# Performance work log

Hardware: AMD Instinct MI355X
Metric: run time of the kernel (lower is better)

Reference implementation:

```python
import jax, jax.numpy as jnp
import numpy as np
import math

B, S, D, H = 4, 2048, 1024, 16
HD = D // H  # 64
MOD_DIMS = [("text", 768, 2048), ("image", 1024, 1024), ("audio", 512, 1500), ("video", 2048, 512)]
M = len(MOD_DIMS)
WIN, DEPTH = 3, 8


def _cantor_routes():
    coords = []
    for i in range(M):
        x = i / max(1, M - 1)
        x = max(1e-06, min(x, 1.0 - 1e-06))
        val, f = 0.0, 0.5
        for _ in range(DEPTH):
            x *= 3.0
            d = int(x)
            x -= d
            if d == 2:
                val += f
            f *= 0.5
        coords.append(val)
    c = np.asarray(coords, dtype=np.float32)
    dist = np.abs(c[:, None] - c[None, :])
    # topk smallest distances (stable tie-break like torch ascending sort)
    return np.argsort(dist, axis=1, kind="stable")[:, :WIN]

ROUTES = jnp.asarray(_cantor_routes())


def setup_inputs() -> dict:
    key = jax.random.key(0)
    ks = iter(jax.random.split(key, 32))
    inp = {}
    for name, dim, sl in MOD_DIMS:
        inp[name] = jax.random.normal(next(ks), (B, sl, dim), dtype=jnp.float32)
        inp[f"W_{name}"] = jax.random.normal(next(ks), (D, dim), dtype=jnp.float32) / math.sqrt(dim)
        inp[f"b_{name}"] = jnp.zeros((D,), dtype=jnp.float32)
    inp["mod_emb"] = jax.random.normal(next(ks), (M, D), dtype=jnp.float32) * 0.02
    for nm in ("q", "k", "v", "o"):
        inp[f"W{nm}"] = jax.random.normal(next(ks), (D, D), dtype=jnp.float32) / math.sqrt(D)
        inp[f"b{nm}"] = jnp.zeros((D,), dtype=jnp.float32)
    inp["temperature"] = jnp.asarray(0.07, dtype=jnp.float32)
    return inp


def reference(text, image, audio, video, W_text, b_text, W_image, b_image,
              W_audio, b_audio, W_video, b_video, mod_emb, Wq, bq, Wk, bk,
              Wv, bv, Wo, bo, temperature):
    xs = [text, image, audio, video]
    Ws = [W_text, W_image, W_audio, W_video]
    bs = [b_text, b_image, b_audio, b_video]
    projected = []
    for i in range(M):
        p = xs[i] @ Ws[i].T + bs[i] + mod_emb[i]          # [B, s_i, D]
        p = jnp.pad(p, ((0, 0), (0, S - p.shape[1]), (0, 0)))
        projected.append(p)
    stacked = jnp.stack(projected, axis=1)                # [B, M, S, D]

    def heads(x, W, b):
        return (x @ W.T + b).reshape(B, M, S, H, HD).transpose(0, 3, 1, 2, 4)  # [B,H,M,S,HD]

    Q = heads(stacked, Wq, bq)
    K = heads(stacked, Wk, bk)
    V = heads(stacked, Wv, bv)

    Kn = K[:, :, ROUTES]
    Vn = V[:, :, ROUTES]
    scores = jnp.einsum('bhmsd,bhmwsd->bhmsw', Q, Kn) / (math.sqrt(HD) * jnp.abs(temperature))
    attn = jax.nn.softmax(scores, axis=-1)                # dropout is identity at eval
    out = jnp.einsum('bhmsw,bhmwsd->bhmsd', attn, Vn)     # [B,H,M,S,HD]
    fused = out.mean(axis=2)                              # [B,H,S,HD]
    fused = fused.transpose(0, 2, 1, 3).reshape(B, S, D)
    return fused @ Wo.T + bo
```

## Files before the change

kernel.cpp:

```cpp
#include <hip/hip_runtime.h>

typedef unsigned short u16;
typedef __bf16 bf16x8 __attribute__((ext_vector_type(8)));
typedef u16   u16x8  __attribute__((ext_vector_type(8)));
typedef u16   u16x4  __attribute__((ext_vector_type(4)));
typedef float f32x4  __attribute__((ext_vector_type(4)));

#define RPB 5084
#define SL0 2048
#define SL1 1024
#define SL2 1500
#define SL3 512

__device__ __forceinline__ u16 f2bf(float f) {
  union { float f; unsigned u; } x; x.f = f;
  unsigned u = x.u;
  u += 0x7fffu + ((u >> 16) & 1u);
  return (u16)(u >> 16);
}
__device__ __forceinline__ float bf2f(u16 h) {
  union { unsigned u; float f; } x; x.u = ((unsigned)h) << 16;
  return x.f;
}
__device__ __forceinline__ void gll16(const u16* g, u16* l) {
  __builtin_amdgcn_global_load_lds(
      (const __attribute__((address_space(1))) void*)g,
      (__attribute__((address_space(3))) void*)l, 16, 0, 0);
}


#define NSEG 8
struct CvtSegs {
  const float* src[NSEG];
  u16*         dst[NSEG];
  int          blk_end[NSEG];
  int          blk_base[NSEG];
};
__global__ __launch_bounds__(256) void cvt_multi(CvtSegs segs) {
  int blk = blockIdx.x, seg = 0;
#pragma unroll
  for (int s = 0; s < NSEG; ++s) if (blk >= segs.blk_end[s]) seg = s + 1;
  const float* src = segs.src[seg];
  u16* dst = segs.dst[seg];
  int i = (blk - segs.blk_base[seg]) * 1024 + threadIdx.x * 4;
  f32x4 v = *(const f32x4*)(src + i);
  u16x4 o;
  o[0] = f2bf(v[0]); o[1] = f2bf(v[1]); o[2] = f2bf(v[2]); o[3] = f2bf(v[3]);
  *(u16x4*)(dst + i) = o;
}

struct TrSegs { const float* src[4]; u16* dst[4]; int dimc[4]; int blk_end[4]; };
__global__ __launch_bounds__(256) void cvt_transpose(TrSegs ts) {
  __shared__ float t[32][33];
  int blk = blockIdx.x, seg = 0;
#pragma unroll
  for (int s = 0; s < 3; ++s) if (blk >= ts.blk_end[s]) seg = s + 1;
  int base  = seg ? ts.blk_end[seg - 1] : 0;
  int local = blk - base;
  int DIMc  = ts.dimc[seg];
  int tpr   = DIMc >> 5;
  int tr = local / tpr, tc = local - tr * tpr;
  const float* src = ts.src[seg];
  u16* dst = ts.dst[seg];
  int r0 = tr * 32, c0 = tc * 32;
  int cx = threadIdx.x & 31, ry = threadIdx.x >> 5;
#pragma unroll
  for (int k = 0; k < 4; ++k)
    t[ry + 8 * k][cx] = src[(size_t)(r0 + ry + 8 * k) * DIMc + c0 + cx];
  __syncthreads();
#pragma unroll
  for (int k = 0; k < 4; ++k)
    dst[(size_t)(c0 + ry + 8 * k) * 1024 + r0 + cx] = f2bf(t[cx][ry + 8 * k]);
}

__global__ __launch_bounds__(256) void bias_prep(
    const float* __restrict__ Wq, const float* __restrict__ Wk, const float* __restrict__ Wv,
    const float* __restrict__ bq, const float* __restrict__ bk, const float* __restrict__ bv,
    const float* __restrict__ bm0, const float* __restrict__ bm1,
    const float* __restrict__ bm2, const float* __restrict__ bm3,
    const float* __restrict__ emb, float* __restrict__ out )
{
  const int wid  = blockIdx.x * 4 + (threadIdx.x >> 6);
  const int lane = threadIdx.x & 63;
  const int m = wid / 3072, n = wid - m * 3072;
  const float* wr_ = (n < 1024) ? Wq + (size_t)n * 1024
                   : (n < 2048) ? Wk + (size_t)(n - 1024) * 1024
                                : Wv + (size_t)(n - 2048) * 1024;
  const float  br  = (n < 1024) ? bq[n] : (n < 2048) ? bk[n - 1024] : bv[n - 2048];
  const float* bmp = (m == 0) ? bm0 : (m == 1) ? bm1 : (m == 2) ? bm2 : bm3;
  const float* ep  = emb + (size_t)m * 1024;
  const int k0 = lane * 16;
  float s = 0.f;
#pragma unroll
  for (int i = 0; i < 16; ++i) s += wr_[k0 + i] * (bmp[k0 + i] + ep[k0 + i]);
  s += __shfl_xor(s, 1);  s += __shfl_xor(s, 2);  s += __shfl_xor(s, 4);
  s += __shfl_xor(s, 8);  s += __shfl_xor(s, 16); s += __shfl_xor(s, 32);
  if (lane == 0) out[(size_t)m * 3072 + n] = s + br;
}

struct WpSegs { const u16* Bw[4]; u16* Cout[4]; int Nn[4]; int blk_end[4]; };
__global__ __launch_bounds__(256) void gemm_wprep(WpSegs wsg, const u16* __restrict__ A) {
  int blk = blockIdx.x, seg = 0;
#pragma unroll
  for (int s = 0; s < 3; ++s) if (blk >= wsg.blk_end[s]) seg = s + 1;
  const int base  = seg ? wsg.blk_end[seg - 1] : 0;
  const int local = blk - base;
  const int Nn  = wsg.Nn[seg];
  const int ctm = Nn >> 7;
  const int rt  = local / ctm;
  const int row0 = rt * 128, col0 = (local - rt * ctm) * 128;
  const int K = 1024;
  const u16* Bw = wsg.Bw[seg];
  u16* Cout = wsg.Cout[seg];

  __shared__ u16 lA0[128 * 32], lA1[128 * 32];
  __shared__ u16 lB0[128 * 32], lB1[128 * 32];
  const int tid  = threadIdx.x;
  const int lane = tid & 63;
  const int wave = tid >> 6;
  const int wr   = (wave >> 1) * 64;
  const int wc   = (wave & 1) * 64;

  const int srow = lane >> 2;
  const int soct = (((lane & 3) ^ ((lane >> 3) & 3))) << 3;
  const u16* pA0 = A + (size_t)(row0 + wave * 32 + srow) * K + soct;
  const u16* pA1 = pA0 + (size_t)16 * K;
  const u16* pB0 = Bw + (size_t)(col0 + wave * 32 + srow) * K + soct;
  const u16* pB1 = pB0 + (size_t)16 * K;
  u16* dA0a = &lA0[(wave * 32) * 32];      u16* dA1a = &lA0[(wave * 32 + 16) * 32];
  u16* dA0b = &lA1[(wave * 32) * 32];      u16* dA1b = &lA1[(wave * 32 + 16) * 32];
  u16* dB0a = &lB0[(wave * 32) * 32];      u16* dB1a = &lB0[(wave * 32 + 16) * 32];
  u16* dB0b = &lB1[(wave * 32) * 32];      u16* dB1b = &lB1[(wave * 32 + 16) * 32];

  f32x4 acc[4][4];
#pragma unroll
  for (int i = 0; i < 4; ++i)
#pragma unroll
    for (int j = 0; j < 4; ++j) acc[i][j] = f32x4{0.f, 0.f, 0.f, 0.f};

  const int fr  = lane & 15;
  const int fo  = lane >> 4;
  const int lrd = fr * 32 + (((fo ^ ((fr >> 1) & 3))) << 3);
  const int ca  = (wr >> 4) * 512;
  const int cbb = (wc >> 4) * 512;

  for (int k0 = 0; k0 < K; k0 += 64) {
    __syncthreads();
    gll16(pA0 + k0, dA0a);       gll16(pA1 + k0, dA1a);
    gll16(pB0 + k0, dB0a);       gll16(pB1 + k0, dB1a);
    gll16(pA0 + k0 + 32, dA0b);  gll16(pA1 + k0 + 32, dA1b);
    gll16(pB0 + k0 + 32, dB0b);  gll16(pB1 + k0 + 32, dB1b);
    __syncthreads();

    bf16x8 af[4], bfr[4];
#pragma unroll
    for (int j = 0; j < 4; ++j)
      bfr[j] = *(const bf16x8*)&lB0[cbb + j * 512 + lrd];
#pragma unroll
    for (int i = 0; i < 4; ++i)
      af[i] = *(const bf16x8*)&lA0[ca + i * 512 + lrd];
#pragma unroll
    for (int i = 0; i < 4; ++i)
#pragma unroll
      for (int j = 0; j < 4; ++j)
        acc[i][j] = __builtin_amdgcn_mfma_f32_16x16x32_bf16(af[i], bfr[j], acc[i][j], 0, 0, 0);
#pragma unroll
    for (int j = 0; j < 4; ++j)
      bfr[j] = *(const bf16x8*)&lB1[cbb + j * 512 + lrd];
#pragma unroll
    for (int i = 0; i < 4; ++i)
      af[i] = *(const bf16x8*)&lA1[ca + i * 512 + lrd];
#pragma unroll
    for (int i = 0; i < 4; ++i)
#pragma unroll
      for (int j = 0; j < 4; ++j)
        acc[i][j] = __builtin_amdgcn_mfma_f32_16x16x32_bf16(af[i], bfr[j], acc[i][j], 0, 0, 0);
  }

  const int fc = lane & 15;
  const int rq = (lane >> 4) * 4;
#pragma unroll
  for (int i = 0; i < 4; ++i) {
#pragma unroll
    for (int j = 0; j < 4; ++j) {
      const int gc = col0 + wc + j * 16 + fc;
#pragma unroll
      for (int reg = 0; reg < 4; ++reg) {
        int gr = row0 + wr + i * 16 + rq + reg;
        Cout[(size_t)gr * Nn + gc] = f2bf(acc[i][j][reg]);
      }
    }
  }
}

template<int STORE_F32>
__global__ __launch_bounds__(256) void gemm_lds(
    const u16* __restrict__ A,
    const u16* __restrict__ B0, const u16* __restrict__ B1, const u16* __restrict__ B2,
    const float* __restrict__ c0, const float* __restrict__ c1, const float* __restrict__ c2,
    void* __restrict__ Cout, int Mr, int K, int ldc)
{
  __shared__ u16 lA0[128 * 32], lA1[128 * 32];
  __shared__ u16 lB0[128 * 32], lB1[128 * 32];
  const int tid  = threadIdx.x;
  const int lane = tid & 63;
  const int wave = tid >> 6;
  const int wr   = (wave >> 1) * 64;
  const int wc   = (wave & 1) * 64;
  const int row0 = blockIdx.y * 128;

  const int wsel = blockIdx.x >> 3;
  const int colL = (blockIdx.x & 7) * 128;
  const u16*   Bw   = (wsel == 0) ? B0 : (wsel == 1) ? B1 : B2;
  const float* bias = (wsel == 0) ? c0 : (wsel == 1) ? c1 : c2;

  const int srow = lane >> 2;
  const int soct = (((lane & 3) ^ ((lane >> 3) & 3))) << 3;
  int ra0 = row0 + wave * 32 + srow;      if (ra0 >= Mr) ra0 = Mr - 1;
  int ra1 = row0 + wave * 32 + srow + 16; if (ra1 >= Mr) ra1 = Mr - 1;
  const u16* pA0 = A + (size_t)ra0 * K + soct;
  const u16* pA1 = A + (size_t)ra1 * K + soct;
  const u16* pB0 = Bw + (size_t)(colL + wave * 32 + srow) * K + soct;
  const u16* pB1 = pB0 + (size_t)16 * K;
  u16* dA0a = &lA0[(wave * 32) * 32];      u16* dA1a = &lA0[(wave * 32 + 16) * 32];
  u16* dA0b = &lA1[(wave * 32) * 32];      u16* dA1b = &lA1[(wave * 32 + 16) * 32];
  u16* dB0a = &lB0[(wave * 32) * 32];      u16* dB1a = &lB0[(wave * 32 + 16) * 32];
  u16* dB0b = &lB1[(wave * 32) * 32];      u16* dB1b = &lB1[(wave * 32 + 16) * 32];

  f32x4 acc[4][4];
#pragma unroll
  for (int i = 0; i < 4; ++i)
#pragma unroll
    for (int j = 0; j < 4; ++j) acc[i][j] = f32x4{0.f, 0.f, 0.f, 0.f};

  const int fr  = lane & 15;
  const int fo  = lane >> 4;
  const int lrd = fr * 32 + (((fo ^ ((fr >> 1) & 3))) << 3);
  const int ca  = (wr >> 4) * 512;
  const int cbb = (wc >> 4) * 512;

  for (int k0 = 0; k0 < K; k0 += 64) {
    __syncthreads();
    gll16(pA0 + k0, dA0a);       gll16(pA1 + k0, dA1a);
    gll16(pB0 + k0, dB0a);       gll16(pB1 + k0, dB1a);
    gll16(pA0 + k0 + 32, dA0b);  gll16(pA1 + k0 + 32, dA1b);
    gll16(pB0 + k0 + 32, dB0b);  gll16(pB1 + k0 + 32, dB1b);
    __syncthreads();

    bf16x8 af[4], bfr[4];
#pragma unroll
    for (int j = 0; j < 4; ++j)
      bfr[j] = *(const bf16x8*)&lB0[cbb + j * 512 + lrd];
#pragma unroll
    for (int i = 0; i < 4; ++i)
      af[i] = *(const bf16x8*)&lA0[ca + i * 512 + lrd];
#pragma unroll
    for (int i = 0; i < 4; ++i)
#pragma unroll
      for (int j = 0; j < 4; ++j)
        acc[i][j] = __builtin_amdgcn_mfma_f32_16x16x32_bf16(af[i], bfr[j], acc[i][j], 0, 0, 0);
#pragma unroll
    for (int j = 0; j < 4; ++j)
      bfr[j] = *(const bf16x8*)&lB1[cbb + j * 512 + lrd];
#pragma unroll
    for (int i = 0; i < 4; ++i)
      af[i] = *(const bf16x8*)&lA1[ca + i * 512 + lrd];
#pragma unroll
    for (int i = 0; i < 4; ++i)
#pragma unroll
      for (int j = 0; j < 4; ++j)
        acc[i][j] = __builtin_amdgcn_mfma_f32_16x16x32_bf16(af[i], bfr[j], acc[i][j], 0, 0, 0);
  }

  const int fc = lane & 15;
  const int rq = (lane >> 4) * 4;
#pragma unroll
  for (int i = 0; i < 4; ++i) {
#pragma unroll
    for (int j = 0; j < 4; ++j) {
      const int cl = wc + j * 16 + fc;
      const float badd = bias[colL + cl];
      const int gc = blockIdx.x * 128 + cl;
#pragma unroll
      for (int reg = 0; reg < 4; ++reg) {
        int gr = row0 + wr + i * 16 + rq + reg;
        if (gr < Mr) {
          float v = acc[i][j][reg] + badd;
          if (STORE_F32) ((float*)Cout)[(size_t)gr * ldc + gc] = v;
          else           ((u16*)Cout)[(size_t)gr * ldc + gc] = f2bf(v);
        }
      }
    }
  }
}

struct QkvSegs {
  const u16*   A[4];
  const u16*   Bw[4];
  const float* bias[4];
  int Mr[4], K[4], sl[4], obase[4], blk_end[4];
};
__global__ __launch_bounds__(512, 2) void gemm_qkv_seg(QkvSegs qs, u16* __restrict__ C) {
  __shared__ u16 lds[4][2][8192];
  int blk = blockIdx.x, seg = 0;
#pragma unroll
  for (int s = 0; s < 3; ++s) if (blk >= qs.blk_end[s]) seg = s + 1;
  const int base  = seg ? qs.blk_end[seg - 1] : 0;
  const int local = blk - base;
  const int cbt   = local % 12;
  const int row0  = (local / 12) * 256;
  const int colL  = cbt * 256;
  const int Mr = qs.Mr[seg], K = qs.K[seg], sl = qs.sl[seg], obase = qs.obase[seg];
  const u16* A  = qs.A[seg];
  const u16* Bw = qs.Bw[seg];
  const float* bias = qs.bias[seg];

  const int tid  = threadIdx.x;
  const int lane = tid & 63;
  const int wave = tid >> 6;
  const int wm   = wave >> 2;
  const int wn   = wave & 3;

  const int srow = lane >> 2;
  const int soct = (((lane & 3) ^ ((lane >> 3) & 3))) << 3;
  int ra0 = row0 + wave * 16 + srow;        if (ra0 >= Mr) ra0 = Mr - 1;
  int ra1 = row0 + 128 + wave * 16 + srow;  if (ra1 >= Mr) ra1 = Mr - 1;
  const u16* pA0 = A + (size_t)ra0 * K + soct;
  const u16* pA1 = A + (size_t)ra1 * K + soct;
  const u16* pB0 = Bw + (size_t)(colL + wave * 16 + srow) * K + soct;
  const u16* pB1 = pB0 + (size_t)128 * K;
  const int NS = K >> 5;

#define QSTAGE(slot, k0) do {                                   \
    gll16(pA0 + (k0), (u16*)&lds[slot][0][wave * 512]);         \
    gll16(pA1 + (k0), (u16*)&lds[slot][0][4096 + wave * 512]);  \
    gll16(pB0 + (k0), (u16*)&lds[slot][1][wave * 512]);         \
    gll16(pB1 + (k0), (u16*)&lds[slot][1][4096 + wave * 512]);  \
  } while (0)

  f32x4 acc[8][4];
#pragma unroll
  for (int m = 0; m < 8; ++m)
#pragma unroll
    for (int n = 0; n < 4; ++n) acc[m][n] = f32x4{0.f, 0.f, 0.f, 0.f};

  QSTAGE(0, 0);
  QSTAGE(1, 32);
  QSTAGE(2, 64);

  const int fr  = lane & 15;
  const int fo  = lane >> 4;
  const int lrd = fr * 32 + (((fo ^ ((fr >> 1) & 3))) << 3);
  const int cam = wm * 8 * 512;
  const int cbn = wn * 4 * 512;

#pragma unroll 4
  for (int s = 0; s < NS; ++s) {
    asm volatile("s_waitcnt vmcnt(8)" ::: "memory");
    __builtin_amdgcn_s_barrier();
    asm volatile("" ::: "memory");

    const u16* Ab = &lds[s & 3][0][0];
    const u16* Bb = &lds[s & 3][1][0];
    bf16x8 af[8], bf[4];
#pragma unroll
    for (int n = 0; n < 4; ++n)
      bf[n] = *(const bf16x8*)&Bb[cbn + n * 512 + lrd];
#pragma unroll
    for (int m = 0; m < 8; ++m)
      af[m] = *(const bf16x8*)&Ab[cam + m * 512 + lrd];

    const int s3 = s + 3;
    const int k3 = (s3 < NS ? s3 : NS - 1) << 5;
    QSTAGE(s3 & 3, k3);

#pragma unroll
    for (int m = 0; m < 8; ++m)
#pragma unroll
      for (int n = 0; n < 4; ++n)
        acc[m][n] = __builtin_amdgcn_mfma_f32_16x16x32_bf16(af[m], bf[n], acc[m][n], 0, 0, 0);
  }
#undef QSTAGE

  asm volatile("s_waitcnt vmcnt(0)" ::: "memory");

  const int fc = lane & 15;
  const int rq = (lane >> 4) * 4;
#pragma unroll
  for (int m = 0; m < 8; ++m) {
#pragma unroll
    for (int n = 0; n < 4; ++n) {
      const int cl = wn * 64 + n * 16 + fc;
      const float badd = bias[colL + cl];
      const int gc = colL + cl;
#pragma unroll
      for (int reg = 0; reg < 4; ++reg) {
        int gr = row0 + wm * 128 + m * 16 + rq + reg;
        if (gr < Mr) {
          int bb = gr / sl, ss = gr - bb * sl;
          C[(size_t)(bb * RPB + obase + ss) * 3072 + gc] = f2bf(acc[m][n][reg] + badd);
        }
      }
    }
  }
}

__global__ __launch_bounds__(256) void attn_fuse(
    const u16* __restrict__ QKV,
    u16* __restrict__ fused,
    const float* __restrict__ bq, const float* __restrict__ bk, const float* __restrict__ bv,
    const float* __restrict__ temp_ptr)
{
  const int ROUTE[4][3] = {{0,1,2},{0,1,2},{2,3,0},{3,2,0}};
  const int SLm[4]  = {SL0, SL1, SL2, SL3};
  const int OFFS[4] = {0, 2048, 3072, 4572};
  const int tid  = threadIdx.x;
  const int lane = tid & 63;
  const int wave = tid >> 6;
  const int bs   = blockIdx.x * 2 + (wave >> 1);
  const int s    = bs & 2047;
  const int b    = bs >> 11;
  const int h    = (wave & 1) * 8 + (lane >> 3);
  const int sub  = lane & 7;
  const int dbase = h * 64 + sub * 8;
  const float scale = 1.0f / (8.0f * fabsf(temp_ptr[0]));

  float qf[4][8], kf[4][8], vf[4][8];
#pragma unroll
  for (int r = 0; r < 4; ++r) {
    if (s < SLm[r]) {
      const u16* base = QKV + ((size_t)(b * RPB + OFFS[r] + s)) * 3072 + dbase;
      u16x8 q8 = *(const u16x8*)(base);
      u16x8 k8 = *(const u16x8*)(base + 1024);
      u16x8 v8 = *(const u16x8*)(base + 2048);
#pragma unroll
      for (int i = 0; i < 8; ++i) {
        qf[r][i] = bf2f(q8[i]); kf[r][i] = bf2f(k8[i]); vf[r][i] = bf2f(v8[i]);
      }
    } else {
#pragma unroll
      for (int i = 0; i < 8; ++i) {
        qf[r][i] = bq[dbase + i]; kf[r][i] = bk[dbase + i]; vf[r][i] = bv[dbase + i];
      }
    }
  }

  float acc[8];
#pragma unroll
  for (int i = 0; i < 8; ++i) acc[i] = 0.f;

#pragma unroll
  for (int m = 0; m < 4; ++m) {
    float sc[3];
#pragma unroll
    for (int w = 0; w < 3; ++w) {
      const int r = ROUTE[m][w];
      float d = 0.f;
#pragma unroll
      for (int i = 0; i < 8; ++i) d += qf[m][i] * kf[r][i];
      d += __shfl_xor(d, 1, 64);
      d += __shfl_xor(d, 2, 64);
      d += __shfl_xor(d, 4, 64);
      sc[w] = d * scale;
    }
    float mx = fmaxf(sc[0], fmaxf(sc[1], sc[2]));
    float e0 = __expf(sc[0] - mx), e1 = __expf(sc[1] - mx), e2 = __expf(sc[2] - mx);
    float inv = 1.0f / (e0 + e1 + e2);
    float ws[3] = {e0 * inv, e1 * inv, e2 * inv};
#pragma unroll
    for (int w = 0; w < 3; ++w) {
      const int r = ROUTE[m][w];
#pragma unroll
      for (int i = 0; i < 8; ++i) acc[i] += ws[w] * vf[r][i];
    }
  }
  u16x8 o;
#pragma unroll
  for (int i = 0; i < 8; ++i) o[i] = f2bf(acc[i] * 0.25f);
  *(u16x8*)(fused + (size_t)bs * 1024 + dbase) = o;
}

extern "C" void kernel_launch(void* const* d_in, const int* in_sizes, int n_in,
                              void* d_out, int out_size, void* d_ws, size_t ws_size,
                              hipStream_t stream) {
  const int B = 4, S = 2048, D = 1024;
  const int SL[4]   = {SL0, SL1, SL2, SL3};
  const int DIM[4]  = {768, 1024, 512, 2048};
  const int OFFS[4] = {0, 2048, 3072, 4572};

  const float* x[4]  = {(const float*)d_in[0], (const float*)d_in[3], (const float*)d_in[6], (const float*)d_in[9]};
  const float* Wm[4] = {(const float*)d_in[1], (const float*)d_in[4], (const float*)d_in[7], (const float*)d_in[10]};
  const float* bm[4] = {(const float*)d_in[2], (const float*)d_in[5], (const float*)d_in[8], (const float*)d_in[11]};
  const float* mod_emb = (const float*)d_in[12];
  const float* Wq = (const float*)d_in[13]; const float* bq = (const float*)d_in[14];
  const float* Wk = (const float*)d_in[15]; const float* bk = (const float*)d_in[16];
  const float* Wv = (const float*)d_in[17]; const float* bv = (const float*)d_in[18];
  const float* Wo = (const float*)d_in[19]; const float* bo = (const float*)d_in[20];
  const float* temp = (const float*)d_in[21];

  const int RROWS = B * RPB;
  const size_t qkvB   = ((size_t)RROWS * 3 * D * 2 + 255) / 256 * 256;
  size_t xbB[4], wmTB[4], wqkvmB[4];
  size_t xbTot = 0, wmTTot = 0, wqkvmTot = 0;
  for (int m = 0; m < 4; ++m) {
    xbB[m]    = ((size_t)B * SL[m] * DIM[m] * 2 + 255) / 256 * 256;  xbTot    += xbB[m];
    wmTB[m]   = ((size_t)DIM[m] * D * 2 + 255) / 256 * 256;          wmTTot   += wmTB[m];
    wqkvmB[m] = ((size_t)3 * D * DIM[m] * 2 + 255) / 256 * 256;      wqkvmTot += wqkvmB[m];
  }
  const size_t wB   = (size_t)D * D * 2;
  const size_t bqmB = ((size_t)4 * 3 * D * 4 + 255) / 256 * 256;
  const size_t need = qkvB + xbTot + wmTTot + 3 * wB + wB + wqkvmTot + bqmB;
  if (ws_size < need) return;

  char* p = (char*)d_ws;
  u16* qkv = (u16*)p;  p += qkvB;
  u16* xb[4];
  char* xbBase = p;
  for (int m = 0; m < 4; ++m) { xb[m] = (u16*)p; p += xbB[m]; }
  u16* wmT[4];
  for (int m = 0; m < 4; ++m) { wmT[m] = (u16*)p; p += wmTB[m]; }
  u16* wqb = (u16*)p;  p += wB;
  u16* wkb = (u16*)p;  p += wB;
  u16* wvb = (u16*)p;  p += wB;
  u16* wob = (u16*)p;  p += wB;
  u16* wqkvm[4];
  for (int m = 0; m < 4; ++m) { wqkvm[m] = (u16*)p; p += wqkvmB[m]; }
  float* bqm = (float*)p;  p += bqmB;
  u16* fusedb = (u16*)xbBase;

  {
    CvtSegs cs;
    const float* srcs[NSEG] = {x[0], x[1], x[2], x[3], Wq, Wk, Wv, Wo};
    u16* dsts[NSEG] = {xb[0], xb[1], xb[2], xb[3], wqb, wkb, wvb, wob};
    int ns[NSEG];
    for (int m = 0; m < 4; ++m) ns[m] = B * SL[m] * DIM[m];
    for (int i = 0; i < 4; ++i) ns[4 + i] = D * D;
    int base = 0;
    for (int i = 0; i < NSEG; ++i) {
      cs.src[i] = srcs[i]; cs.dst[i] = dsts[i];
      cs.blk_base[i] = base;
      base += (ns[i] + 1023) / 1024;
      cs.blk_end[i] = base;
    }
    cvt_multi<<<base, 256, 0, stream>>>(cs);
  }

  {
    TrSegs ts;
    int base = 0;
    for (int m = 0; m < 4; ++m) {
      ts.src[m] = Wm[m]; ts.dst[m] = wmT[m]; ts.dimc[m] = DIM[m];
      base += (D / 32) * (DIM[m] / 32);
      ts.blk_end[m] = base;
    }
    cvt_transpose<<<base, 256, 0, stream>>>(ts);
  }

  bias_prep<<<3072, 256, 0, stream>>>(Wq, Wk, Wv, bq, bk, bv,
                                      bm[0], bm[1], bm[2], bm[3], mod_emb, bqm);

  {
    const int ord[4] = {3, 1, 0, 2};
    WpSegs wsg;
    int base = 0;
    for (int i = 0; i < 4; ++i) {
      int m = ord[i];
      wsg.Bw[i] = wmT[m]; wsg.Cout[i] = wqkvm[m]; wsg.Nn[i] = DIM[m];
      base += (3 * D / 128) * (DIM[m] / 128);
      wsg.blk_end[i] = base;
    }
    gemm_wprep<<<base, 256, 0, stream>>>(wsg, wqb);
  }

  {
    const int ord[4] = {3, 1, 0, 2};
    QkvSegs qsg;
    int base = 0;
    for (int i = 0; i < 4; ++i) {
      int m = ord[i];
      int Mr = B * SL[m];
      qsg.A[i] = xb[m]; qsg.Bw[i] = wqkvm[m]; qsg.bias[i] = bqm + m * 3072;
      qsg.Mr[i] = Mr; qsg.K[i] = DIM[m]; qsg.sl[i] = SL[m]; qsg.obase[i] = OFFS[m];
      base += 12 * ((Mr + 255) / 256);
      qsg.blk_end[i] = base;
    }
    gemm_qkv_seg<<<base, 512, 0, stream>>>(qsg, qkv);
  }

  attn_fuse<<<(B * S) / 2, 256, 0, stream>>>(qkv, fusedb, bq, bk, bv, temp);

  {
    dim3 grid(8, (B * S) / 128);
    gemm_lds<1><<<grid, 256, 0, stream>>>(fusedb, wob, wob, wob, bo, bo, bo,
                                          d_out, B * S, D, D);
  }
}
```

Before: 469.7 us.

## Merge prep kernels into one launch and run QKV GEMM with 1024-thread blocks

Three preprocessing kernels (fp32→bf16 conversion, weight transpose, bias folding) become one segmented launch, removing two kernel launches and the gaps between them. The QKV GEMM keeps its 256x256 tile but now uses 16 waves of 1024 threads. Each wave owns a 64x64 sub-tile and issues half as many global→LDS loads per stage, which cuts per-thread accumulators and registers. The epilogue computes the batch/sequence split once per wave instead of dividing per element. The risk is that 1024-thread blocks with 64KB of LDS allow fewer resident blocks per CU and add barrier cost, which may weaken latency hiding in the pipelined K loop.

```diff
diff --git a/kernel.cpp b/kernel.cpp
--- a/kernel.cpp
+++ b/kernel.cpp
@@ -29,73 +29,69 @@
 }
 
 
-#define NSEG 8
-struct CvtSegs {
-  const float* src[NSEG];
-  u16*         dst[NSEG];
-  int          blk_end[NSEG];
-  int          blk_base[NSEG];
+struct PrepAll {
+  const float* csrc[8]; u16* cdst[8]; int cend[8]; int cbase[8];
+  const float* tsrc[4]; u16* tdst[4]; int tdim[4]; int tend[4];
+  const float *Wq, *Wk, *Wv, *bq, *bk, *bv, *bm0, *bm1, *bm2, *bm3, *emb;
+  float* bout;
+  int cvtN, trN;
 };
-__global__ __launch_bounds__(256) void cvt_multi(CvtSegs segs) {
-  int blk = blockIdx.x, seg = 0;
-#pragma unroll
-  for (int s = 0; s < NSEG; ++s) if (blk >= segs.blk_end[s]) seg = s + 1;
-  const float* src = segs.src[seg];
-  u16* dst = segs.dst[seg];
-  int i = (blk - segs.blk_base[seg]) * 1024 + threadIdx.x * 4;
-  f32x4 v = *(const f32x4*)(src + i);
-  u16x4 o;
-  o[0] = f2bf(v[0]); o[1] = f2bf(v[1]); o[2] = f2bf(v[2]); o[3] = f2bf(v[3]);
-  *(u16x4*)(dst + i) = o;
-}
-
-struct TrSegs { const float* src[4]; u16* dst[4]; int dimc[4]; int blk_end[4]; };
-__global__ __launch_bounds__(256) void cvt_transpose(TrSegs ts) {
+__global__ __launch_bounds__(256) void prep_all(PrepAll pa) {
   __shared__ float t[32][33];
-  int blk = blockIdx.x, seg = 0;
-#pragma unroll
-  for (int s = 0; s < 3; ++s) if (blk >= ts.blk_end[s]) seg = s + 1;
-  int base  = seg ? ts.blk_end[seg - 1] : 0;
-  int local = blk - base;
-  int DIMc  = ts.dimc[seg];
-  int tpr   = DIMc >> 5;
-  int tr = local / tpr, tc = local - tr * tpr;
-  const float* src = ts.src[seg];
-  u16* dst = ts.dst[seg];
-  int r0 = tr * 32, c0 = tc * 32;
-  int cx = threadIdx.x & 31, ry = threadIdx.x >> 5;
-#pragma unroll
-  for (int k = 0; k < 4; ++k)
-    t[ry + 8 * k][cx] = src[(size_t)(r0 + ry + 8 * k) * DIMc + c0 + cx];
-  __syncthreads();
-#pragma unroll
-  for (int k = 0; k < 4; ++k)
-    dst[(size_t)(c0 + ry + 8 * k) * 1024 + r0 + cx] = f2bf(t[cx][ry + 8 * k]);
-}
-
-__global__ __launch_bounds__(256) void bias_prep(
-    const float* __restrict__ Wq, const float* __restrict__ Wk, const float* __restrict__ Wv,
-    const float* __restrict__ bq, const float* __restrict__ bk, const float* __restrict__ bv,
-    const float* __restrict__ bm0, const float* __restrict__ bm1,
-    const float* __restrict__ bm2, const float* __restrict__ bm3,
-    const float* __restrict__ emb, float* __restrict__ out )
-{
-  const int wid  = blockIdx.x * 4 + (threadIdx.x >> 6);
+  int blk = blockIdx.x;
+  if (blk < pa.cvtN) {
+    int seg = 0;
+#pragma unroll
+    for (int s = 0; s < 8; ++s) if (blk >= pa.cend[s]) seg = s + 1;
+    const float* src = pa.csrc[seg];
+    u16* dst = pa.cdst[seg];
+    int i = (blk - pa.cbase[seg]) * 1024 + threadIdx.x * 4;
+    f32x4 v = *(const f32x4*)(src + i);
+    u16x4 o;
+    o[0] = f2bf(v[0]); o[1] = f2bf(v[1]); o[2] = f2bf(v[2]); o[3] = f2bf(v[3]);
+    *(u16x4*)(dst + i) = o;
+    return;
+  }
+  blk -= pa.cvtN;
+  if (blk < pa.trN) {
+    int seg = 0;
+#pragma unroll
+    for (int s = 0; s < 3; ++s) if (blk >= pa.tend[s]) seg = s + 1;
+    int base  = seg ? pa.tend[seg - 1] : 0;
+    int local = blk - base;
+    int DIMc  = pa.tdim[seg];
+    int tpr   = DIMc >> 5;
+    int tr = local / tpr, tc = local - tr * tpr;
+    const float* src = pa.tsrc[seg];
+    u16* dst = pa.tdst[seg];
+    int r0 = tr * 32, c0 = tc * 32;
+    int cx = threadIdx.x & 31, ry = threadIdx.x >> 5;
+#pragma unroll
+    for (int k = 0; k < 4; ++k)
+      t[ry + 8 * k][cx] = src[(size_t)(r0 + ry + 8 * k) * DIMc + c0 + cx];
+    __syncthreads();
+#pragma unroll
+    for (int k = 0; k < 4; ++k)
+      dst[(size_t)(c0 + ry + 8 * k) * 1024 + r0 + cx] = f2bf(t[cx][ry + 8 * k]);
+    return;
+  }
+  blk -= pa.trN;
+  const int wid  = blk * 4 + (threadIdx.x >> 6);
   const int lane = threadIdx.x & 63;
   const int m = wid / 3072, n = wid - m * 3072;
-  const float* wr_ = (n < 1024) ? Wq + (size_t)n * 1024
-                   : (n < 2048) ? Wk + (size_t)(n - 1024) * 1024
-                                : Wv + (size_t)(n - 2048) * 1024;
-  const float  br  = (n < 1024) ? bq[n] : (n < 2048) ? bk[n - 1024] : bv[n - 2048];
-  const float* bmp = (m == 0) ? bm0 : (m == 1) ? bm1 : (m == 2) ? bm2 : bm3;
-  const float* ep  = emb + (size_t)m * 1024;
+  const float* wr_ = (n < 1024) ? pa.Wq + (size_t)n * 1024
+                   : (n < 2048) ? pa.Wk + (size_t)(n - 1024) * 1024
+                                : pa.Wv + (size_t)(n - 2048) * 1024;
+  const float  br  = (n < 1024) ? pa.bq[n] : (n < 2048) ? pa.bk[n - 1024] : pa.bv[n - 2048];
+  const float* bmp = (m == 0) ? pa.bm0 : (m == 1) ? pa.bm1 : (m == 2) ? pa.bm2 : pa.bm3;
+  const float* ep  = pa.emb + (size_t)m * 1024;
   const int k0 = lane * 16;
   float s = 0.f;
 #pragma unroll
   for (int i = 0; i < 16; ++i) s += wr_[k0 + i] * (bmp[k0 + i] + ep[k0 + i]);
   s += __shfl_xor(s, 1);  s += __shfl_xor(s, 2);  s += __shfl_xor(s, 4);
   s += __shfl_xor(s, 8);  s += __shfl_xor(s, 16); s += __shfl_xor(s, 32);
-  if (lane == 0) out[(size_t)m * 3072 + n] = s + br;
+  if (lane == 0) pa.bout[(size_t)m * 3072 + n] = s + br;
 }
 
 struct WpSegs { const u16* Bw[4]; u16* Cout[4]; int Nn[4]; int blk_end[4]; };
@@ -300,7 +296,7 @@
   const float* bias[4];
   int Mr[4], K[4], sl[4], obase[4], blk_end[4];
 };
-__global__ __launch_bounds__(512, 2) void gemm_qkv_seg(QkvSegs qs, u16* __restrict__ C) {
+__global__ __launch_bounds__(1024) void gemm_qkv_seg(QkvSegs qs, u16* __restrict__ C) {
   __shared__ u16 lds[4][2][8192];
   int blk = blockIdx.x, seg = 0;
 #pragma unroll
@@ -323,24 +319,19 @@
 
   const int srow = lane >> 2;
   const int soct = (((lane & 3) ^ ((lane >> 3) & 3))) << 3;
-  int ra0 = row0 + wave * 16 + srow;        if (ra0 >= Mr) ra0 = Mr - 1;
-  int ra1 = row0 + 128 + wave * 16 + srow;  if (ra1 >= Mr) ra1 = Mr - 1;
-  const u16* pA0 = A + (size_t)ra0 * K + soct;
-  const u16* pA1 = A + (size_t)ra1 * K + soct;
-  const u16* pB0 = Bw + (size_t)(colL + wave * 16 + srow) * K + soct;
-  const u16* pB1 = pB0 + (size_t)128 * K;
+  int ra = row0 + wave * 16 + srow;  if (ra >= Mr) ra = Mr - 1;
+  const u16* pA = A + (size_t)ra * K + soct;
+  const u16* pB = Bw + (size_t)(colL + wave * 16 + srow) * K + soct;
   const int NS = K >> 5;
 
-#define QSTAGE(slot, k0) do {                                   \
-    gll16(pA0 + (k0), (u16*)&lds[slot][0][wave * 512]);         \
-    gll16(pA1 + (k0), (u16*)&lds[slot][0][4096 + wave * 512]);  \
-    gll16(pB0 + (k0), (u16*)&lds[slot][1][wave * 512]);         \
-    gll16(pB1 + (k0), (u16*)&lds[slot][1][4096 + wave * 512]);  \
+#define QSTAGE(slot, k0) do {                               \
+    gll16(pA + (k0), (u16*)&lds[slot][0][wave * 512]);      \
+    gll16(pB + (k0), (u16*)&lds[slot][1][wave * 512]);      \
   } while (0)
 
-  f32x4 acc[8][4];
-#pragma unroll
-  for (int m = 0; m < 8; ++m)
+  f32x4 acc[4][4];
+#pragma unroll
+  for (int m = 0; m < 4; ++m)
 #pragma unroll
     for (int n = 0; n < 4; ++n) acc[m][n] = f32x4{0.f, 0.f, 0.f, 0.f};
 
@@ -351,23 +342,23 @@
   const int fr  = lane & 15;
   const int fo  = lane >> 4;
   const int lrd = fr * 32 + (((fo ^ ((fr >> 1) & 3))) << 3);
-  const int cam = wm * 8 * 512;
+  const int cam = wm * 4 * 512;
   const int cbn = wn * 4 * 512;
 
 #pragma unroll 4
   for (int s = 0; s < NS; ++s) {
-    asm volatile("s_waitcnt vmcnt(8)" ::: "memory");
+    asm volatile("s_waitcnt vmcnt(4)" ::: "memory");
     __builtin_amdgcn_s_barrier();
     asm volatile("" ::: "memory");
 
     const u16* Ab = &lds[s & 3][0][0];
     const u16* Bb = &lds[s & 3][1][0];
-    bf16x8 af[8], bf[4];
+    bf16x8 af[4], bf[4];
 #pragma unroll
     for (int n = 0; n < 4; ++n)
       bf[n] = *(const bf16x8*)&Bb[cbn + n * 512 + lrd];
 #pragma unroll
-    for (int m = 0; m < 8; ++m)
+    for (int m = 0; m < 4; ++m)
       af[m] = *(const bf16x8*)&Ab[cam + m * 512 + lrd];
 
     const int s3 = s + 3;
@@ -375,7 +366,7 @@
     QSTAGE(s3 & 3, k3);
 
 #pragma unroll
-    for (int m = 0; m < 8; ++m)
+    for (int m = 0; m < 4; ++m)
 #pragma unroll
       for (int n = 0; n < 4; ++n)
         acc[m][n] = __builtin_amdgcn_mfma_f32_16x16x32_bf16(af[m], bf[n], acc[m][n], 0, 0, 0);
@@ -386,8 +377,11 @@
 
   const int fc = lane & 15;
   const int rq = (lane >> 4) * 4;
-#pragma unroll
-  for (int m = 0; m < 8; ++m) {
+  const int u0  = row0 + wm * 64;
+  const int bb0 = u0 / sl;
+  const int ss0 = u0 - bb0 * sl;
+#pragma unroll
+  for (int m = 0; m < 4; ++m) {
 #pragma unroll
     for (int n = 0; n < 4; ++n) {
       const int cl = wn * 64 + n * 16 + fc;
@@ -395,9 +389,10 @@
       const int gc = colL + cl;
 #pragma unroll
       for (int reg = 0; reg < 4; ++reg) {
-        int gr = row0 + wm * 128 + m * 16 + rq + reg;
-        if (gr < Mr) {
-          int bb = gr / sl, ss = gr - bb * sl;
+        const int off = m * 16 + rq + reg;
+        if (u0 + off < Mr) {
+          int ss = ss0 + off, bb = bb0;
+          if (ss >= sl) { ss -= sl; ++bb; }
           C[(size_t)(bb * RPB + obase + ss) * 3072 + gc] = f2bf(acc[m][n][reg] + badd);
         }
       }
@@ -529,35 +524,33 @@
   u16* fusedb = (u16*)xbBase;
 
   {
-    CvtSegs cs;
-    const float* srcs[NSEG] = {x[0], x[1], x[2], x[3], Wq, Wk, Wv, Wo};
-    u16* dsts[NSEG] = {xb[0], xb[1], xb[2], xb[3], wqb, wkb, wvb, wob};
-    int ns[NSEG];
+    PrepAll pa;
+    const float* csrcs[8] = {x[0], x[1], x[2], x[3], Wq, Wk, Wv, Wo};
+    u16* cdsts[8] = {xb[0], xb[1], xb[2], xb[3], wqb, wkb, wvb, wob};
+    int ns[8];
     for (int m = 0; m < 4; ++m) ns[m] = B * SL[m] * DIM[m];
     for (int i = 0; i < 4; ++i) ns[4 + i] = D * D;
-    int base = 0;
-    for (int i = 0; i < NSEG; ++i) {
-      cs.src[i] = srcs[i]; cs.dst[i] = dsts[i];
-      cs.blk_base[i] = base;
-      base += (ns[i] + 1023) / 1024;
-      cs.blk_end[i] = base;
-    }
-    cvt_multi<<<base, 256, 0, stream>>>(cs);
-  }
-
-  {
-    TrSegs ts;
-    int base = 0;
+    int cbase = 0;
+    for (int i = 0; i < 8; ++i) {
+      pa.csrc[i] = csrcs[i]; pa.cdst[i] = cdsts[i];
+      pa.cbase[i] = cbase;
+      cbase += (ns[i] + 1023) / 1024;
+      pa.cend[i] = cbase;
+    }
+    pa.cvtN = cbase;
+    int tb = 0;
     for (int m = 0; m < 4; ++m) {
-      ts.src[m] = Wm[m]; ts.dst[m] = wmT[m]; ts.dimc[m] = DIM[m];
-      base += (D / 32) * (DIM[m] / 32);
-      ts.blk_end[m] = base;
-    }
-    cvt_transpose<<<base, 256, 0, stream>>>(ts);
-  }
-
-  bias_prep<<<3072, 256, 0, stream>>>(Wq, Wk, Wv, bq, bk, bv,
-                                      bm[0], bm[1], bm[2], bm[3], mod_emb, bqm);
+      pa.tsrc[m] = Wm[m]; pa.tdst[m] = wmT[m]; pa.tdim[m] = DIM[m];
+      tb += (D / 32) * (DIM[m] / 32);
+      pa.tend[m] = tb;
+    }
+    pa.trN = tb;
+    pa.Wq = Wq; pa.Wk = Wk; pa.Wv = Wv;
+    pa.bq = bq; pa.bk = bk; pa.bv = bv;
+    pa.bm0 = bm[0]; pa.bm1 = bm[1]; pa.bm2 = bm[2]; pa.bm3 = bm[3];
+    pa.emb = mod_emb; pa.bout = bqm;
+    prep_all<<<pa.cvtN + pa.trN + 3072, 256, 0, stream>>>(pa);
+  }
 
   {
     const int ord[4] = {3, 1, 0, 2};
@@ -584,7 +577,7 @@
       base += 12 * ((Mr + 255) / 256);
       qsg.blk_end[i] = base;
     }
-    gemm_qkv_seg<<<base, 512, 0, stream>>>(qsg, qkv);
+    gemm_qkv_seg<<<base, 1024, 0, stream>>>(qsg, qkv);
   }
 
   attn_fuse<<<(B * S) / 2, 256, 0, stream>>>(qkv, fusedb, bq, bk, bv, temp);
```

Result: faster. 419.5 us (-10.7%).
